# Optimization experiments

Measured on AMD Instinct MI355X. Metric: run time of the kernel, lower is better.

## Reference

```python
import jax, jax.numpy as jnp
import numpy as np


def setup_inputs() -> dict:
    key = jax.random.key(0)
    k1, k2 = jax.random.split(key)
    B, C = 8388608, 3
    outputs = jax.random.normal(k1, (B, C), dtype=jnp.float32)
    targets = jax.random.uniform(k2, (B, C), dtype=jnp.float32)
    return {"outputs": outputs, "targets": targets}


def reference(outputs, targets):
    B = outputs.shape[0]
    # Columns 1 and 2 are periodic angles in [0, 1).
    o_ang = outputs[:, 1:3]
    t_ang = targets[:, 1:3]
    # constant penalty: |out // 1| summed over batch and both angle cols, / B
    constant_penalty = jnp.sum(jnp.abs(jnp.floor(o_ang))) / B
    # wrap outputs into [0, 1)
    o_wrapped = jnp.mod(o_ang, 1.0)
    # if |o - t| > 0.5, shift target toward output by +/-1 (wrap-around)
    shift = jnp.where(t_ang < o_wrapped, 1.0, -1.0)
    t_shifted = jnp.where(jnp.abs(o_wrapped - t_ang) > 0.5, t_ang + shift, t_ang)
    out_full = outputs.at[:, 1:3].set(o_wrapped)
    tgt_full = targets.at[:, 1:3].set(t_shifted)
    mse = jnp.mean((out_full - tgt_full) ** 2)
    return mse + constant_penalty
```

## Files before the change

kernel.cpp:

```cpp
#include <hip/hip_runtime.h>


constexpr int BLOCK = 256;
constexpr int F4T = 8;
constexpr int F4_PER_BLOCK = BLOCK * F4T;

__device__ inline void elem(float oo, float tt, bool ang, float& sq, float& pen) {
    const float fl = floorf(oo);
    const float ow = oo - fl;
    const float shift = (tt < ow) ? 1.0f : -1.0f;
    const float ts = (fabsf(ow - tt) > 0.5f) ? (tt + shift) : tt;
    const float da = ow - ts;
    const float dl = oo - tt;
    const float d = ang ? da : dl;
    sq = fmaf(d, d, sq);
    pen += ang ? fabsf(fl) : 0.0f;
}

__device__ inline void proc4(const float4 o, const float4 t, int im,
                             float& sq, float& pen) {
    elem(o.x, t.x, im != 0, sq, pen);
    const int c1 = (im == 2) ? 0 : im + 1;
    elem(o.y, t.y, c1 != 0, sq, pen);
    const int c2 = (c1 == 2) ? 0 : c1 + 1;
    elem(o.z, t.z, c2 != 0, sq, pen);
    const int c3 = (c2 == 2) ? 0 : c2 + 1;
    elem(o.w, t.w, c3 != 0, sq, pen);
}

__global__ __launch_bounds__(BLOCK) void bcmse_partial(
    const float* __restrict__ outs,
    const float* __restrict__ tgts,
    long long n,
    float2* __restrict__ partials)
{
    const long long n4 = n >> 2;
    const long long base = (long long)blockIdx.x * F4_PER_BLOCK + threadIdx.x;

    const float4* __restrict__ o4 = reinterpret_cast<const float4*>(outs);
    const float4* __restrict__ t4 = reinterpret_cast<const float4*>(tgts);

    long long idx[F4T];
    bool g[F4T];
    #pragma unroll
    for (int k = 0; k < F4T; ++k) {
        const long long i = base + (long long)k * BLOCK;
        g[k] = i < n4;
        idx[k] = g[k] ? i : 0;
    }

    float4 ov[F4T], tv[F4T];
    #pragma unroll
    for (int k = 0; k < F4T; ++k) ov[k] = o4[idx[k]];
    #pragma unroll
    for (int k = 0; k < F4T; ++k) tv[k] = t4[idx[k]];

    int im = (int)(base % 3);

    float sq = 0.f, pen = 0.f;
    #pragma unroll
    for (int k = 0; k < F4T; ++k) {
        float s = 0.f, p = 0.f;
        proc4(ov[k], tv[k], im, s, p);
        if (g[k]) { sq += s; pen += p; }
        im = (im == 2) ? 0 : im + 1;
    }

    if (blockIdx.x == 0 && threadIdx.x == 0) {
        for (long long e = n4 * 4; e < n; ++e) {
            elem(outs[e], tgts[e], (e % 3) != 0, sq, pen);
        }
    }

    #pragma unroll
    for (int off = 32; off > 0; off >>= 1) {
        sq  += __shfl_down(sq,  off, 64);
        pen += __shfl_down(pen, off, 64);
    }

    __shared__ float s_sq[BLOCK / 64], s_pen[BLOCK / 64];
    const int lane = threadIdx.x & 63;
    const int wave = threadIdx.x >> 6;
    if (lane == 0) { s_sq[wave] = sq; s_pen[wave] = pen; }
    __syncthreads();

    if (threadIdx.x == 0) {
        float bsq = 0.f, bpen = 0.f;
        #pragma unroll
        for (int w = 0; w < BLOCK / 64; ++w) { bsq += s_sq[w]; bpen += s_pen[w]; }
        partials[blockIdx.x] = make_float2(bsq, bpen);
    }
}

__global__ __launch_bounds__(BLOCK) void bcmse_reduce(
    const float2* __restrict__ partials, int nblocks,
    float* __restrict__ out, double invN, double invB)
{
    double dsq = 0.0, dpen = 0.0;
    for (int k = threadIdx.x; k < nblocks; k += BLOCK) {
        const float2 p = partials[k];
        dsq  += (double)p.x;
        dpen += (double)p.y;
    }
    #pragma unroll
    for (int off = 32; off > 0; off >>= 1) {
        dsq  += __shfl_down(dsq,  off, 64);
        dpen += __shfl_down(dpen, off, 64);
    }
    __shared__ double r_sq[BLOCK / 64], r_pen[BLOCK / 64];
    const int lane = threadIdx.x & 63;
    const int wave = threadIdx.x >> 6;
    if (lane == 0) { r_sq[wave] = dsq; r_pen[wave] = dpen; }
    __syncthreads();
    if (threadIdx.x == 0) {
        double fsq = 0.0, fpen = 0.0;
        #pragma unroll
        for (int w = 0; w < BLOCK / 64; ++w) { fsq += r_sq[w]; fpen += r_pen[w]; }
        out[0] = (float)(fsq * invN + fpen * invB);
    }
}

extern "C" void kernel_launch(void* const* d_in, const int* in_sizes, int n_in,
                              void* d_out, int out_size, void* d_ws, size_t ws_size,
                              hipStream_t stream) {
    const float* outs = (const float*)d_in[0];
    const float* tgts = (const float*)d_in[1];
    float* out = (float*)d_out;
    float2* partials = (float2*)d_ws;

    const long long n = (long long)in_sizes[0];
    const long long n4 = n >> 2;
    const int nblocks = (int)((n4 + F4_PER_BLOCK - 1) / F4_PER_BLOCK);
    const double invN = 1.0 / (double)n;
    const double invB = 3.0 / (double)n;

    bcmse_partial<<<nblocks, BLOCK, 0, stream>>>(outs, tgts, n, partials);
    bcmse_reduce<<<1, BLOCK, 0, stream>>>(partials, nblocks, out, invN, invB);
}
```

Measured before the change: 38.83 us.

## Fuse final reduction into partial kernel via last-block atomic counter

Replaces the separate single-block reduce kernel with a last-block-done pattern. Each block atomically stores its packed partial and increments a counter, and the block that arrives last sums all partials and writes the result. This removes one kernel launch and the gap between kernels, but adds a hipMemsetAsync on the counter plus atomic and serialization overhead in the final block.

```diff
diff --git a/kernel.cpp b/kernel.cpp
--- a/kernel.cpp
+++ b/kernel.cpp
@@ -28,11 +28,14 @@
     elem(o.w, t.w, c3 != 0, sq, pen);
 }
 
-__global__ __launch_bounds__(BLOCK) void bcmse_partial(
+__global__ __launch_bounds__(BLOCK) void bcmse_fused(
     const float* __restrict__ outs,
     const float* __restrict__ tgts,
     long long n,
-    float2* __restrict__ partials)
+    unsigned long long* __restrict__ partials,
+    unsigned* __restrict__ counter,
+    float* __restrict__ out,
+    double invN, double invB)
 {
     const long long n4 = n >> 2;
     const long long base = (long long)blockIdx.x * F4_PER_BLOCK + threadIdx.x;
@@ -79,6 +82,7 @@
     }
 
     __shared__ float s_sq[BLOCK / 64], s_pen[BLOCK / 64];
+    __shared__ bool s_last;
     const int lane = threadIdx.x & 63;
     const int wave = threadIdx.x >> 6;
     if (lane == 0) { s_sq[wave] = sq; s_pen[wave] = pen; }
@@ -88,35 +92,40 @@
         float bsq = 0.f, bpen = 0.f;
         #pragma unroll
         for (int w = 0; w < BLOCK / 64; ++w) { bsq += s_sq[w]; bpen += s_pen[w]; }
-        partials[blockIdx.x] = make_float2(bsq, bpen);
+        union { float2 f; unsigned long long u; } pk;
+        pk.f = make_float2(bsq, bpen);
+        __hip_atomic_store(&partials[blockIdx.x], pk.u,
+                           __ATOMIC_RELAXED, __HIP_MEMORY_SCOPE_AGENT);
+        const unsigned prev = __hip_atomic_fetch_add(counter, 1u,
+                           __ATOMIC_ACQ_REL, __HIP_MEMORY_SCOPE_AGENT);
+        s_last = (prev == gridDim.x - 1);
     }
-}
+    __syncthreads();
 
-__global__ __launch_bounds__(BLOCK) void bcmse_reduce(
-    const float2* __restrict__ partials, int nblocks,
-    float* __restrict__ out, double invN, double invB)
-{
-    double dsq = 0.0, dpen = 0.0;
-    for (int k = threadIdx.x; k < nblocks; k += BLOCK) {
-        const float2 p = partials[k];
-        dsq  += (double)p.x;
-        dpen += (double)p.y;
-    }
-    #pragma unroll
-    for (int off = 32; off > 0; off >>= 1) {
-        dsq  += __shfl_down(dsq,  off, 64);
-        dpen += __shfl_down(dpen, off, 64);
-    }
-    __shared__ double r_sq[BLOCK / 64], r_pen[BLOCK / 64];
-    const int lane = threadIdx.x & 63;
-    const int wave = threadIdx.x >> 6;
-    if (lane == 0) { r_sq[wave] = dsq; r_pen[wave] = dpen; }
-    __syncthreads();
-    if (threadIdx.x == 0) {
-        double fsq = 0.0, fpen = 0.0;
+    if (s_last) {
+        double dsq = 0.0, dpen = 0.0;
+        const int nb = (int)gridDim.x;
+        for (int k = threadIdx.x; k < nb; k += BLOCK) {
+            union { float2 f; unsigned long long u; } pk;
+            pk.u = __hip_atomic_load(&partials[k],
+                       __ATOMIC_RELAXED, __HIP_MEMORY_SCOPE_AGENT);
+            dsq  += (double)pk.f.x;
+            dpen += (double)pk.f.y;
+        }
         #pragma unroll
-        for (int w = 0; w < BLOCK / 64; ++w) { fsq += r_sq[w]; fpen += r_pen[w]; }
-        out[0] = (float)(fsq * invN + fpen * invB);
+        for (int off = 32; off > 0; off >>= 1) {
+            dsq  += __shfl_down(dsq,  off, 64);
+            dpen += __shfl_down(dpen, off, 64);
+        }
+        __shared__ double r_sq[BLOCK / 64], r_pen[BLOCK / 64];
+        if (lane == 0) { r_sq[wave] = dsq; r_pen[wave] = dpen; }
+        __syncthreads();
+        if (threadIdx.x == 0) {
+            double fsq = 0.0, fpen = 0.0;
+            #pragma unroll
+            for (int w = 0; w < BLOCK / 64; ++w) { fsq += r_sq[w]; fpen += r_pen[w]; }
+            out[0] = (float)(fsq * invN + fpen * invB);
+        }
     }
 }
 
@@ -126,7 +135,6 @@
     const float* outs = (const float*)d_in[0];
     const float* tgts = (const float*)d_in[1];
     float* out = (float*)d_out;
-    float2* partials = (float2*)d_ws;
 
     const long long n = (long long)in_sizes[0];
     const long long n4 = n >> 2;
@@ -134,6 +142,11 @@
     const double invN = 1.0 / (double)n;
     const double invB = 3.0 / (double)n;
 
-    bcmse_partial<<<nblocks, BLOCK, 0, stream>>>(outs, tgts, n, partials);
-    bcmse_reduce<<<1, BLOCK, 0, stream>>>(partials, nblocks, out, invN, invB);
+    unsigned long long* partials = (unsigned long long*)d_ws;
+    unsigned* counter = (unsigned*)((char*)d_ws + (size_t)nblocks * 8);
+
+    hipMemsetAsync(counter, 0, sizeof(unsigned), stream);
+
+    bcmse_fused<<<nblocks, BLOCK, 0, stream>>>(outs, tgts, n, partials,
+                                               counter, out, invN, invB);
 }
```

Result: slower. 138.0 us (+255.4%).

## Fuse final reduction into main kernel via atomics and last-block counter

Applied to the files above, without the earlier changes.

Replaces the two-kernel partial/reduce scheme with one kernel. Each block atomically adds its double-precision partial sums into a global accumulator and increments a counter, and the last block writes the final result. This removes the second kernel launch and the partials round trip. In exchange it adds a memset before the launch and contended double atomics across about 12K blocks, so the summation order is no longer deterministic.

```diff
diff --git a/kernel.cpp b/kernel.cpp
--- a/kernel.cpp
+++ b/kernel.cpp
@@ -28,11 +28,14 @@
     elem(o.w, t.w, c3 != 0, sq, pen);
 }
 
-__global__ __launch_bounds__(BLOCK) void bcmse_partial(
+__global__ __launch_bounds__(BLOCK) void bcmse_fused(
     const float* __restrict__ outs,
     const float* __restrict__ tgts,
     long long n,
-    float2* __restrict__ partials)
+    double* __restrict__ acc,
+    unsigned* __restrict__ counter,
+    float* __restrict__ out,
+    double invN, double invB)
 {
     const long long n4 = n >> 2;
     const long long base = (long long)blockIdx.x * F4_PER_BLOCK + threadIdx.x;
@@ -88,35 +91,20 @@
         float bsq = 0.f, bpen = 0.f;
         #pragma unroll
         for (int w = 0; w < BLOCK / 64; ++w) { bsq += s_sq[w]; bpen += s_pen[w]; }
-        partials[blockIdx.x] = make_float2(bsq, bpen);
-    }
-}
 
-__global__ __launch_bounds__(BLOCK) void bcmse_reduce(
-    const float2* __restrict__ partials, int nblocks,
-    float* __restrict__ out, double invN, double invB)
-{
-    double dsq = 0.0, dpen = 0.0;
-    for (int k = threadIdx.x; k < nblocks; k += BLOCK) {
-        const float2 p = partials[k];
-        dsq  += (double)p.x;
-        dpen += (double)p.y;
-    }
-    #pragma unroll
-    for (int off = 32; off > 0; off >>= 1) {
-        dsq  += __shfl_down(dsq,  off, 64);
-        dpen += __shfl_down(dpen, off, 64);
-    }
-    __shared__ double r_sq[BLOCK / 64], r_pen[BLOCK / 64];
-    const int lane = threadIdx.x & 63;
-    const int wave = threadIdx.x >> 6;
-    if (lane == 0) { r_sq[wave] = dsq; r_pen[wave] = dpen; }
-    __syncthreads();
-    if (threadIdx.x == 0) {
-        double fsq = 0.0, fpen = 0.0;
-        #pragma unroll
-        for (int w = 0; w < BLOCK / 64; ++w) { fsq += r_sq[w]; fpen += r_pen[w]; }
-        out[0] = (float)(fsq * invN + fpen * invB);
+        atomicAdd(&acc[0], (double)bsq);
+        atomicAdd(&acc[1], (double)bpen);
+        asm volatile("s_waitcnt vmcnt(0)" ::: "memory");
+        const unsigned prev = __hip_atomic_fetch_add(
+            counter, 1u, __ATOMIC_RELAXED, __HIP_MEMORY_SCOPE_AGENT);
+
+        if (prev == gridDim.x - 1) {
+            const double fsq = __hip_atomic_fetch_add(
+                &acc[0], 0.0, __ATOMIC_RELAXED, __HIP_MEMORY_SCOPE_AGENT);
+            const double fpen = __hip_atomic_fetch_add(
+                &acc[1], 0.0, __ATOMIC_RELAXED, __HIP_MEMORY_SCOPE_AGENT);
+            out[0] = (float)(fsq * invN + fpen * invB);
+        }
     }
 }
 
@@ -126,7 +114,6 @@
     const float* outs = (const float*)d_in[0];
     const float* tgts = (const float*)d_in[1];
     float* out = (float*)d_out;
-    float2* partials = (float2*)d_ws;
 
     const long long n = (long long)in_sizes[0];
     const long long n4 = n >> 2;
@@ -134,6 +121,11 @@
     const double invN = 1.0 / (double)n;
     const double invB = 3.0 / (double)n;
 
-    bcmse_partial<<<nblocks, BLOCK, 0, stream>>>(outs, tgts, n, partials);
-    bcmse_reduce<<<1, BLOCK, 0, stream>>>(partials, nblocks, out, invN, invB);
+    double* acc = (double*)d_ws;
+    unsigned* counter = (unsigned*)((char*)d_ws + 16);
+
+    hipMemsetAsync(d_ws, 0, 24, stream);
+
+    bcmse_fused<<<nblocks, BLOCK, 0, stream>>>(outs, tgts, n, acc,
+                                               counter, out, invN, invB);
 }
```

Measured after the change: 133.3 us. 243% more time.
